# Kernel tuning notes

Measured on AMD Instinct MI355X. Metric: run time of the kernel, lower is better.

## Reference

```python
import jax, jax.numpy as jnp
import numpy as np

NUM_HEADS = 16
NUM_KV_HEADS = 2
HEAD_DIM = 256
HIDDEN = 2048
ROT_DIM = 64          # head_dim * partial_rotary_factor (0.25)
ROPE_THETA = 10000.0
EPS = 1e-6
T = 4096


def setup_inputs() -> dict:
    key = jax.random.key(0)
    k1, k2, k3, k4, k5 = jax.random.split(key, 5)
    qkv_out = HEAD_DIM * (NUM_HEADS * 2 + 2 * NUM_KV_HEADS)  # 9216 (q+gate, k, v)
    return {
        "hidden_states": jax.random.normal(k1, (T, HIDDEN), dtype=jnp.float32),
        "positions": jnp.arange(T, dtype=jnp.int32),
        "w_qkv": jax.random.normal(k2, (HIDDEN, qkv_out), dtype=jnp.float32) * 0.02,
        "w_o": jax.random.normal(k3, (NUM_HEADS * HEAD_DIM, HIDDEN), dtype=jnp.float32) * 0.02,
        "q_norm_w": jax.random.normal(k4, (HEAD_DIM,), dtype=jnp.float32) * 0.1,
        "k_norm_w": jax.random.normal(k5, (HEAD_DIM,), dtype=jnp.float32) * 0.1,
    }


def _gemma_rmsnorm(x, w):
    # GemmaRMSNorm: fp32 compute, scale by (1 + weight)
    xf = x.astype(jnp.float32)
    xf = xf * jax.lax.rsqrt(jnp.mean(xf * xf, axis=-1, keepdims=True) + EPS)
    return (xf * (1.0 + w.astype(jnp.float32))).astype(x.dtype)


def _apply_rope(x, positions):
    # neox-style partial RoPE on first ROT_DIM dims; x: [T, H, D]
    half = ROT_DIM // 2
    inv_freq = 1.0 / (ROPE_THETA ** (jnp.arange(0, ROT_DIM, 2, dtype=jnp.float32) / ROT_DIM))
    freqs = positions.astype(jnp.float32)[:, None] * inv_freq  # [T, half]
    cos = jnp.cos(freqs)[:, None, :]  # [T, 1, half]
    sin = jnp.sin(freqs)[:, None, :]
    x1 = x[..., :half]
    x2 = x[..., half:ROT_DIM]
    rot = jnp.concatenate([x1 * cos - x2 * sin, x2 * cos + x1 * sin], axis=-1)
    return jnp.concatenate([rot, x[..., ROT_DIM:]], axis=-1)


def reference(hidden_states, positions, w_qkv, w_o, q_norm_w, k_norm_w):
    q_size = NUM_HEADS * HEAD_DIM
    kv_size = NUM_KV_HEADS * HEAD_DIM
    qkv = hidden_states @ w_qkv  # [T, 2*q_size + 2*kv_size]

    # split q+gate (interleaved per head), k, v
    q_gate = qkv[:, : 2 * q_size].reshape(-1, NUM_HEADS, 2 * HEAD_DIM)
    q = q_gate[..., :HEAD_DIM]          # [T, H, D]
    gate = q_gate[..., HEAD_DIM:]       # [T, H, D]
    k = qkv[:, 2 * q_size : 2 * q_size + kv_size].reshape(-1, NUM_KV_HEADS, HEAD_DIM)
    v = qkv[:, 2 * q_size + kv_size :].reshape(-1, NUM_KV_HEADS, HEAD_DIM)

    # per-head QK RMSNorm then partial RoPE
    q = _apply_rope(_gemma_rmsnorm(q, q_norm_w), positions)
    k = _apply_rope(_gemma_rmsnorm(k, k_norm_w), positions)

    # GQA causal attention
    rep = NUM_HEADS // NUM_KV_HEADS
    k_rep = jnp.repeat(k, rep, axis=1)  # [T, H, D]
    v_rep = jnp.repeat(v, rep, axis=1)
    scaling = HEAD_DIM ** -0.5
    scores = jnp.einsum("qhd,khd->hqk", q, k_rep) * scaling  # [H, T, T]
    causal = positions[:, None] >= positions[None, :]
    scores = jnp.where(causal[None, :, :], scores, jnp.finfo(scores.dtype).min)
    probs = jax.nn.softmax(scores, axis=-1)
    attn = jnp.einsum("hqk,khd->qhd", probs, v_rep)  # [T, H, D]

    # sigmoid-gated output, then O projection
    attn = attn * jax.nn.sigmoid(gate)
    return attn.reshape(-1, NUM_HEADS * HEAD_DIM) @ w_o
```

## Files before the change

kernel.cpp:

```cpp
#include <hip/hip_runtime.h>

typedef __attribute__((ext_vector_type(4))) float f32x4;
typedef __attribute__((ext_vector_type(8))) __bf16 bf16x8;
typedef unsigned short ushort_t;
typedef unsigned int uint_t;
typedef __attribute__((ext_vector_type(4))) uint_t u32x4;

__device__ __forceinline__ float bf2f(ushort_t u) {
  union { uint_t i; float f; } v; v.i = ((uint_t)u) << 16; return v.f;
}
__device__ __forceinline__ ushort_t f2bf(float f) {
  union { float f; uint_t i; } v; v.f = f;
  uint_t x = v.i;
  return (ushort_t)((x + 0x7fffu + ((x >> 16) & 1u)) >> 16);
}

__device__ __forceinline__ void gload_lds16(const void* g, void* l) {
  __builtin_amdgcn_global_load_lds(
      (const __attribute__((address_space(1))) void*)g,
      (__attribute__((address_space(3))) void*)l, 16, 0, 0);
}

__global__ __launch_bounds__(256) void cast_bf16_kernel(
    const float* __restrict__ in, ushort_t* __restrict__ out, int n8) {
  int i = blockIdx.x * 256 + threadIdx.x;
  if (i >= n8) return;
  float4 a = ((const float4*)in)[i * 2];
  float4 b = ((const float4*)in)[i * 2 + 1];
  ushort4 o0 = make_ushort4(f2bf(a.x), f2bf(a.y), f2bf(a.z), f2bf(a.w));
  ushort4 o1 = make_ushort4(f2bf(b.x), f2bf(b.y), f2bf(b.z), f2bf(b.w));
  ((ushort4*)out)[i * 2] = o0;
  ((ushort4*)out)[i * 2 + 1] = o1;
}

__global__ __launch_bounds__(256) void transpose_cast_kernel(
    const float* __restrict__ in, ushort_t* __restrict__ out, int R, int C) {
  __shared__ float tile[32][33];
  int tx = threadIdx.x, ty = threadIdx.y;
  int c0 = blockIdx.x * 32, r0 = blockIdx.y * 32;
#pragma unroll
  for (int i = 0; i < 4; ++i)
    tile[ty + i * 8][tx] = in[(size_t)(r0 + ty + i * 8) * C + c0 + tx];
  __syncthreads();
#pragma unroll
  for (int i = 0; i < 4; ++i)
    out[(size_t)(c0 + ty + i * 8) * R + r0 + tx] = f2bf(tile[tx][ty + i * 8]);
}

template <int OUT_BF16>
__global__ __launch_bounds__(256, 2) void gemm_bt_kernel(
    const ushort_t* __restrict__ A, const ushort_t* __restrict__ BT,
    void* __restrict__ Cout, int M, int N, int K, int nx, int cpx) {
  const int lin = blockIdx.x;
  const int swz = (lin & 7) * cpx + (lin >> 3);
  const int bx = swz % nx, by = swz / nx;

  __shared__ ushort_t As[128 * 32];
  __shared__ ushort_t Bs[128 * 32];
  const int tid = threadIdx.x;
  const int lane = tid & 63;
  const int wid = tid >> 6;
  const int wr = wid >> 1, wc = wid & 1;
  const int qr = lane & 15, kg = lane >> 4;
  const size_t arow = (size_t)by * 128;
  const size_t brow = (size_t)bx * 128;

  f32x4 acc[4][4] = {};

  for (int k0 = 0; k0 < K; k0 += 32) {
    __syncthreads();
#pragma unroll
    for (int t = 0; t < 2; ++t) {
      int c = (t * 4 + wid) * 64 + lane;
      int r = c >> 2, kc = (c & 3) * 8;
      gload_lds16(A + (arow + r) * K + k0 + kc, &As[(t * 4 + wid) * 512]);
      gload_lds16(BT + (brow + r) * K + k0 + kc, &Bs[(t * 4 + wid) * 512]);
    }
    __syncthreads();
    bf16x8 af[4], bfr[4];
#pragma unroll
    for (int m = 0; m < 4; ++m)
      af[m] = *(const bf16x8*)&As[(wr * 64 + m * 16 + qr) * 32 + kg * 8];
#pragma unroll
    for (int n = 0; n < 4; ++n)
      bfr[n] = *(const bf16x8*)&Bs[(wc * 64 + n * 16 + qr) * 32 + kg * 8];
#pragma unroll
    for (int m = 0; m < 4; ++m)
#pragma unroll
      for (int n = 0; n < 4; ++n)
        acc[m][n] = __builtin_amdgcn_mfma_f32_16x16x32_bf16(af[m], bfr[n], acc[m][n], 0, 0, 0);
  }

#pragma unroll
  for (int m = 0; m < 4; ++m)
#pragma unroll
    for (int n = 0; n < 4; ++n)
#pragma unroll
      for (int j = 0; j < 4; ++j) {
        size_t row = arow + wr * 64 + m * 16 + kg * 4 + j;
        size_t col = brow + wc * 64 + n * 16 + qr;
        float v = acc[m][n][j];
        if (OUT_BF16) ((ushort_t*)Cout)[row * N + col] = f2bf(v);
        else ((float*)Cout)[row * N + col] = v;
      }
}

__global__ __launch_bounds__(256) void normrope_kernel(
    ushort_t* __restrict__ qkv, const int* __restrict__ positions,
    const float* __restrict__ qw, const float* __restrict__ kw) {
  const int wv = blockIdx.x * 4 + (threadIdx.x >> 6);
  const int lane = threadIdx.x & 63;
  const int t = wv / 18;
  const int idx = wv % 18;
  size_t base;
  const float* w;
  float sc;
  if (idx < 16) { base = (size_t)t * 9216 + idx * 512; w = qw; sc = 0.0625f; }
  else { base = (size_t)t * 9216 + 8192 + (size_t)(idx - 16) * 256; w = kw; sc = 1.0f; }

  ushort4 raw = *(const ushort4*)(qkv + base + lane * 4);
  float x0 = bf2f(raw.x), x1 = bf2f(raw.y), x2 = bf2f(raw.z), x3 = bf2f(raw.w);
  float ss = x0 * x0 + x1 * x1 + x2 * x2 + x3 * x3;
#pragma unroll
  for (int off = 1; off < 64; off <<= 1) ss += __shfl_xor(ss, off);
  float inv = rsqrtf(ss * (1.0f / 256.0f) + 1e-6f);
  const int d0 = lane * 4;
  float xn[4] = { x0 * inv * (1.f + w[d0]), x1 * inv * (1.f + w[d0 + 1]),
                  x2 * inv * (1.f + w[d0 + 2]), x3 * inv * (1.f + w[d0 + 3]) };
  float pn[4];
#pragma unroll
  for (int j = 0; j < 4; ++j) pn[j] = __shfl_xor(xn[j], 8);
  if (lane < 16) {
    const float pos = (float)positions[t];
#pragma unroll
    for (int j = 0; j < 4; ++j) {
      int d = d0 + j;
      int i = d & 31;
      float invf = __expf(-(float)i * 0.28782313662425574f);
      float fr = pos * invf;
      float s, c;
      sincosf(fr, &s, &c);
      xn[j] = (d < 32) ? (xn[j] * c - pn[j] * s) : (xn[j] * c + pn[j] * s);
    }
  }
  ushort4 o = make_ushort4(f2bf(xn[0] * sc), f2bf(xn[1] * sc),
                           f2bf(xn[2] * sc), f2bf(xn[3] * sc));
  *(ushort4*)(qkv + base + lane * 4) = o;
}

__device__ __forceinline__ bf16x8 softmax_group(
    f32x4 sA, f32x4 sB, int kv0, int qg, bool full,
    float& mr, float& lr, f32x4* o, int kg) {
  float v[8];
#pragma unroll
  for (int j = 0; j < 4; ++j) v[j] = sA[j];
#pragma unroll
  for (int j = 0; j < 4; ++j) v[4 + j] = sB[j];
  if (!full) {
#pragma unroll
    for (int j = 0; j < 4; ++j) {
      if (kv0 + kg * 4 + j > qg) v[j] = -1e30f;
      if (kv0 + 16 + kg * 4 + j > qg) v[4 + j] = -1e30f;
    }
  }
  float tm = v[0];
#pragma unroll
  for (int j = 1; j < 8; ++j) tm = fmaxf(tm, v[j]);
  tm = fmaxf(tm, __shfl_xor(tm, 16));
  tm = fmaxf(tm, __shfl_xor(tm, 32));
  float mref;
  if (__all(tm - mr <= 8.0f)) {
    mref = mr;
  } else {
    float mnew = fmaxf(mr, tm);
    float corr = __expf(mr - mnew);
    lr *= corr;
    float c0 = __shfl(corr, kg * 4 + 0);
    float c1 = __shfl(corr, kg * 4 + 1);
    float c2 = __shfl(corr, kg * 4 + 2);
    float c3 = __shfl(corr, kg * 4 + 3);
#pragma unroll
    for (int n = 0; n < 16; ++n) {
      o[n][0] *= c0; o[n][1] *= c1; o[n][2] *= c2; o[n][3] *= c3;
    }
    mr = mnew; mref = mnew;
  }
  float p[8];
#pragma unroll
  for (int j = 0; j < 8; ++j) p[j] = __expf(v[j] - mref);
  float ps = 0.f;
#pragma unroll
  for (int j = 0; j < 8; ++j) ps += p[j];
  ps += __shfl_xor(ps, 16);
  ps += __shfl_xor(ps, 32);
  lr += ps;
  union { u32x4 u; bf16x8 b; } pk;
#pragma unroll
  for (int u2 = 0; u2 < 4; ++u2)
    pk.u[u2] = (uint_t)f2bf(p[u2]) | ((uint_t)f2bf(p[4 + u2]) << 16);
  return pk.b;
}

__global__ __launch_bounds__(256, 1) void attn_kernel(
    const ushort_t* __restrict__ qkv, ushort_t* __restrict__ A2) {
  const int id = blockIdx.x;
  const int g8 = id & 255, k8 = id >> 8;
  const int t8 = g8 >> 4;
  const int h = ((g8 & 1) << 3) | ((g8 >> 1) & 7);
  const int qt = k8 ? (15 - t8) : (16 + t8);
  const int kvh = g8 & 1;
  const int tid = threadIdx.x;
  const int lane = tid & 63;
  const int wid = tid >> 6;
  const int qr = lane & 15, kg = lane >> 4;

  __shared__ __align__(16) ushort_t Ks[2][32 * 256];
  __shared__ __align__(16) ushort_t Vt[2][256 * 32];

  const int q0 = qt * 128;
  const int myq0 = q0 + wid * 32;

  bf16x8 qf[2][8];
#pragma unroll
  for (int g = 0; g < 2; ++g)
#pragma unroll
    for (int kd = 0; kd < 8; ++kd)
      qf[g][kd] = *(const bf16x8*)(qkv + (size_t)(myq0 + g * 16 + qr) * 9216 +
                                   h * 512 + kd * 32 + kg * 8);

  f32x4 o0[16] = {}, o1[16] = {};
  float mr0 = -1e30f, mr1 = -1e30f, lr0 = 0.f, lr1 = 0.f;

  const int nt = qt * 4 + 4;

  u32x4 vlo0, vhi0, vlo1, vhi1;
  const int vr = tid & 15;
  const int vd0 = (tid >> 4) * 8;
  const int vd1 = vd0 + 128;

#pragma unroll
  for (int t = 0; t < 4; ++t) {
    int c = (t * 4 + wid) * 64 + lane;
    int r = c >> 5, dc = c & 31;
    int dcs = dc ^ (r & 7);
    gload_lds16(qkv + (size_t)r * 9216 + 8192 + kvh * 256 + dcs * 8,
                &Ks[0][(t * 4 + wid) * 512]);
  }
  {
    const ushort_t* g0 = qkv + (size_t)vr * 9216 + 8704 + kvh * 256;
    vlo0 = *(const u32x4*)(g0 + vd0);
    vhi0 = *(const u32x4*)(g0 + 16 * 9216 + vd0);
    vlo1 = *(const u32x4*)(g0 + vd1);
    vhi1 = *(const u32x4*)(g0 + 16 * 9216 + vd1);
  }

  int buf = 0;
  for (int kt = 0; kt < nt; ++kt) {
    const int kv0 = kt * 32;

    {
      char* vbase = (char*)&Vt[buf][0];
#pragma unroll
      for (int half = 0; half < 2; ++half) {
        u32x4 lo = half ? vlo1 : vlo0;
        u32x4 hi = half ? vhi1 : vhi0;
        int dbase = half ? vd1 : vd0;
#pragma unroll
        for (int w = 0; w < 4; ++w) {
          uint_t v0 = (lo[w] & 0xffffu) | (hi[w] << 16);
          uint_t v1 = (lo[w] >> 16) | (hi[w] & 0xffff0000u);
          int d0v = dbase + 2 * w, d1v = d0v + 1;
          int rsw = ((vr >> 2) * 16) + (vr & 3) * 4;
          *(uint_t*)(vbase + (d0v ^ ((d0v >> 3) & 1)) * 64 +
                     (rsw ^ ((d0v & 3) * 16))) = v0;
          *(uint_t*)(vbase + (d1v ^ ((d1v >> 3) & 1)) * 64 +
                     (rsw ^ ((d1v & 3) * 16))) = v1;
        }
      }
    }
    __syncthreads();

    if (kt + 1 < nt) {
      const int kv0n = kv0 + 32;
#pragma unroll
      for (int t = 0; t < 4; ++t) {
        int c = (t * 4 + wid) * 64 + lane;
        int r = c >> 5, dc = c & 31;
        int dcs = dc ^ (r & 7);
        gload_lds16(qkv + (size_t)(kv0n + r) * 9216 + 8192 + kvh * 256 + dcs * 8,
                    &Ks[buf ^ 1][(t * 4 + wid) * 512]);
      }
      const ushort_t* g0 = qkv + (size_t)(kv0n + vr) * 9216 + 8704 + kvh * 256;
      vlo0 = *(const u32x4*)(g0 + vd0);
      vhi0 = *(const u32x4*)(g0 + 16 * 9216 + vd0);
      vlo1 = *(const u32x4*)(g0 + vd1);
      vhi1 = *(const u32x4*)(g0 + 16 * 9216 + vd1);
    }
    __builtin_amdgcn_sched_barrier(0);

    const bool active = (kv0 <= myq0 + 31);
    if (active) {
      const char* ksb = (const char*)&Ks[buf][0];
      const int kxor = (qr & 7) << 4;
      const int kbase = qr * 512;
      f32x4 s00 = {0.f, 0.f, 0.f, 0.f}, s01 = {0.f, 0.f, 0.f, 0.f};
      f32x4 s10 = {0.f, 0.f, 0.f, 0.f}, s11 = {0.f, 0.f, 0.f, 0.f};
      __builtin_amdgcn_s_setprio(1);
#pragma unroll
      for (int kd = 0; kd < 8; ++kd) {
        int off = kbase + ((kd * 64 + kg * 16) ^ kxor);
        bf16x8 kf0 = *(const bf16x8*)(ksb + off);
        bf16x8 kf1 = *(const bf16x8*)(ksb + off + 8192);
        s00 = __builtin_amdgcn_mfma_f32_16x16x32_bf16(kf0, qf[0][kd], s00, 0, 0, 0);
        s01 = __builtin_amdgcn_mfma_f32_16x16x32_bf16(kf0, qf[1][kd], s01, 0, 0, 0);
        s10 = __builtin_amdgcn_mfma_f32_16x16x32_bf16(kf1, qf[0][kd], s10, 0, 0, 0);
        s11 = __builtin_amdgcn_mfma_f32_16x16x32_bf16(kf1, qf[1][kd], s11, 0, 0, 0);
      }
      __builtin_amdgcn_s_setprio(0);

      const bool full = (kv0 + 31 <= myq0);
      bf16x8 pf0 = softmax_group(s00, s10, kv0, myq0 + qr, full, mr0, lr0, o0, kg);
      bf16x8 pf1 = softmax_group(s01, s11, kv0, myq0 + 16 + qr, full, mr1, lr1, o1, kg);

      const char* vtb = (const char*)&Vt[buf][0];
      __builtin_amdgcn_s_setprio(1);
#pragma unroll
      for (int n = 0; n < 16; ++n) {
        int dcol = n * 16 + qr;
        int dsw = dcol ^ ((dcol >> 3) & 1);
        bf16x8 vf = *(const bf16x8*)(vtb + dsw * 64 + ((kg ^ (dcol & 3)) * 16));
        o0[n] = __builtin_amdgcn_mfma_f32_16x16x32_bf16(pf0, vf, o0[n], 0, 0, 0);
        o1[n] = __builtin_amdgcn_mfma_f32_16x16x32_bf16(pf1, vf, o1[n], 0, 0, 0);
      }
      __builtin_amdgcn_s_setprio(0);
    }
    buf ^= 1;
  }

  float rl0[4], rl1[4];
#pragma unroll
  for (int j = 0; j < 4; ++j) {
    rl0[j] = 1.0f / __shfl(lr0, kg * 4 + j);
    rl1[j] = 1.0f / __shfl(lr1, kg * 4 + j);
  }
#pragma unroll
  for (int n = 0; n < 16; ++n) {
    int d = n * 16 + qr;
#pragma unroll
    for (int j = 0; j < 4; ++j) {
      {
        int t = myq0 + kg * 4 + j;
        float val = o0[n][j] * rl0[j];
        float g2 = bf2f(qkv[(size_t)t * 9216 + h * 512 + 256 + d]);
        val *= 1.0f / (1.0f + __expf(-g2));
        A2[(size_t)t * 4096 + h * 256 + d] = f2bf(val);
      }
      {
        int t = myq0 + 16 + kg * 4 + j;
        float val = o1[n][j] * rl1[j];
        float g2 = bf2f(qkv[(size_t)t * 9216 + h * 512 + 256 + d]);
        val *= 1.0f / (1.0f + __expf(-g2));
        A2[(size_t)t * 4096 + h * 256 + d] = f2bf(val);
      }
    }
  }
}

extern "C" void kernel_launch(void* const* d_in, const int* in_sizes, int n_in,
                              void* d_out, int out_size, void* d_ws, size_t ws_size,
                              hipStream_t stream) {
  const float* hidden = (const float*)d_in[0];
  const int* positions = (const int*)d_in[1];
  const float* w_qkv = (const float*)d_in[2];
  const float* w_o = (const float*)d_in[3];
  const float* q_norm_w = (const float*)d_in[4];
  const float* k_norm_w = (const float*)d_in[5];

  char* ws = (char*)d_ws;
  ushort_t* hb    = (ushort_t*)ws;
  ushort_t* wqkvT = (ushort_t*)(ws + 16777216);
  ushort_t* woT   = (ushort_t*)(ws + 54525952);
  ushort_t* qkvb  = (ushort_t*)(ws + 71303168);
  ushort_t* A2    = (ushort_t*)(ws + 146800640);

  hipLaunchKernelGGL(cast_bf16_kernel, dim3(4096), dim3(256), 0, stream,
                     hidden, hb, 1048576);
  hipLaunchKernelGGL(transpose_cast_kernel, dim3(288, 64), dim3(32, 8), 0, stream,
                     w_qkv, wqkvT, 2048, 9216);
  hipLaunchKernelGGL(transpose_cast_kernel, dim3(64, 128), dim3(32, 8), 0, stream,
                     w_o, woT, 4096, 2048);
  hipLaunchKernelGGL((gemm_bt_kernel<1>), dim3(2304), dim3(256), 0, stream,
                     hb, wqkvT, (void*)qkvb, 4096, 9216, 2048, 72, 288);
  hipLaunchKernelGGL(normrope_kernel, dim3(18432), dim3(256), 0, stream,
                     qkvb, positions, q_norm_w, k_norm_w);
  hipLaunchKernelGGL(attn_kernel, dim3(512), dim3(256), 0, stream,
                     qkvb, A2);
  hipLaunchKernelGGL((gemm_bt_kernel<0>), dim3(512), dim3(256), 0, stream,
                     A2, woT, d_out, 4096, 2048, 4096, 16, 64);
}
```

Before: 738.0 us.

## Halve attention query tile to raise occupancy and single-buffer V in LDS

Measured after the change: 913.9 us. 1.24x slower.

```diff
diff --git a/kernel.cpp b/kernel.cpp
--- a/kernel.cpp
+++ b/kernel.cpp
@@ -201,13 +201,13 @@
   return pk.b;
 }
 
-__global__ __launch_bounds__(256, 1) void attn_kernel(
+__global__ __launch_bounds__(256, 3) void attn_kernel(
     const ushort_t* __restrict__ qkv, ushort_t* __restrict__ A2) {
   const int id = blockIdx.x;
-  const int g8 = id & 255, k8 = id >> 8;
-  const int t8 = g8 >> 4;
+  const int g8 = id & 255, kk = id >> 8;
+  const int x = g8 >> 4;
   const int h = ((g8 & 1) << 3) | ((g8 >> 1) & 7);
-  const int qt = k8 ? (15 - t8) : (16 + t8);
+  const int qt = (3 - kk) * 16 + ((kk & 1) ? (15 - x) : x);
   const int kvh = g8 & 1;
   const int tid = threadIdx.x;
   const int lane = tid & 63;
@@ -215,23 +215,21 @@
   const int qr = lane & 15, kg = lane >> 4;
 
   __shared__ __align__(16) ushort_t Ks[2][32 * 256];
-  __shared__ __align__(16) ushort_t Vt[2][256 * 32];
-
-  const int q0 = qt * 128;
-  const int myq0 = q0 + wid * 32;
-
-  bf16x8 qf[2][8];
-#pragma unroll
-  for (int g = 0; g < 2; ++g)
-#pragma unroll
-    for (int kd = 0; kd < 8; ++kd)
-      qf[g][kd] = *(const bf16x8*)(qkv + (size_t)(myq0 + g * 16 + qr) * 9216 +
-                                   h * 512 + kd * 32 + kg * 8);
-
-  f32x4 o0[16] = {}, o1[16] = {};
-  float mr0 = -1e30f, mr1 = -1e30f, lr0 = 0.f, lr1 = 0.f;
-
-  const int nt = qt * 4 + 4;
+  __shared__ __align__(16) ushort_t Vt[256 * 32];
+
+  const int q0 = qt * 64;
+  const int myq0 = q0 + wid * 16;
+
+  bf16x8 qf[8];
+#pragma unroll
+  for (int kd = 0; kd < 8; ++kd)
+    qf[kd] = *(const bf16x8*)(qkv + (size_t)(myq0 + qr) * 9216 + h * 512 +
+                              kd * 32 + kg * 8);
+
+  f32x4 o[16] = {};
+  float mr = -1e30f, lr = 0.f;
+
+  const int nt = qt * 2 + 2;
 
   u32x4 vlo0, vhi0, vlo1, vhi1;
   const int vr = tid & 15;
@@ -259,7 +257,7 @@
     const int kv0 = kt * 32;
 
     {
-      char* vbase = (char*)&Vt[buf][0];
+      char* vbase = (char*)&Vt[0];
 #pragma unroll
       for (int half = 0; half < 2; ++half) {
         u32x4 lo = half ? vlo1 : vlo0;
@@ -298,70 +296,54 @@
     }
     __builtin_amdgcn_sched_barrier(0);
 
-    const bool active = (kv0 <= myq0 + 31);
+    const bool active = (kv0 <= myq0 + 15);
     if (active) {
       const char* ksb = (const char*)&Ks[buf][0];
       const int kxor = (qr & 7) << 4;
       const int kbase = qr * 512;
-      f32x4 s00 = {0.f, 0.f, 0.f, 0.f}, s01 = {0.f, 0.f, 0.f, 0.f};
-      f32x4 s10 = {0.f, 0.f, 0.f, 0.f}, s11 = {0.f, 0.f, 0.f, 0.f};
+      f32x4 s0 = {0.f, 0.f, 0.f, 0.f}, s1 = {0.f, 0.f, 0.f, 0.f};
       __builtin_amdgcn_s_setprio(1);
 #pragma unroll
       for (int kd = 0; kd < 8; ++kd) {
         int off = kbase + ((kd * 64 + kg * 16) ^ kxor);
         bf16x8 kf0 = *(const bf16x8*)(ksb + off);
         bf16x8 kf1 = *(const bf16x8*)(ksb + off + 8192);
-        s00 = __builtin_amdgcn_mfma_f32_16x16x32_bf16(kf0, qf[0][kd], s00, 0, 0, 0);
-        s01 = __builtin_amdgcn_mfma_f32_16x16x32_bf16(kf0, qf[1][kd], s01, 0, 0, 0);
-        s10 = __builtin_amdgcn_mfma_f32_16x16x32_bf16(kf1, qf[0][kd], s10, 0, 0, 0);
-        s11 = __builtin_amdgcn_mfma_f32_16x16x32_bf16(kf1, qf[1][kd], s11, 0, 0, 0);
+        s0 = __builtin_amdgcn_mfma_f32_16x16x32_bf16(kf0, qf[kd], s0, 0, 0, 0);
+        s1 = __builtin_amdgcn_mfma_f32_16x16x32_bf16(kf1, qf[kd], s1, 0, 0, 0);
       }
       __builtin_amdgcn_s_setprio(0);
 
       const bool full = (kv0 + 31 <= myq0);
-      bf16x8 pf0 = softmax_group(s00, s10, kv0, myq0 + qr, full, mr0, lr0, o0, kg);
-      bf16x8 pf1 = softmax_group(s01, s11, kv0, myq0 + 16 + qr, full, mr1, lr1, o1, kg);
-
-      const char* vtb = (const char*)&Vt[buf][0];
+      bf16x8 pf = softmax_group(s0, s1, kv0, myq0 + qr, full, mr, lr, o, kg);
+
+      const char* vtb = (const char*)&Vt[0];
       __builtin_amdgcn_s_setprio(1);
 #pragma unroll
       for (int n = 0; n < 16; ++n) {
         int dcol = n * 16 + qr;
         int dsw = dcol ^ ((dcol >> 3) & 1);
         bf16x8 vf = *(const bf16x8*)(vtb + dsw * 64 + ((kg ^ (dcol & 3)) * 16));
-        o0[n] = __builtin_amdgcn_mfma_f32_16x16x32_bf16(pf0, vf, o0[n], 0, 0, 0);
-        o1[n] = __builtin_amdgcn_mfma_f32_16x16x32_bf16(pf1, vf, o1[n], 0, 0, 0);
+        o[n] = __builtin_amdgcn_mfma_f32_16x16x32_bf16(pf, vf, o[n], 0, 0, 0);
       }
       __builtin_amdgcn_s_setprio(0);
     }
+    __syncthreads();
     buf ^= 1;
   }
 
-  float rl0[4], rl1[4];
-#pragma unroll
-  for (int j = 0; j < 4; ++j) {
-    rl0[j] = 1.0f / __shfl(lr0, kg * 4 + j);
-    rl1[j] = 1.0f / __shfl(lr1, kg * 4 + j);
-  }
+  float rl[4];
+#pragma unroll
+  for (int j = 0; j < 4; ++j) rl[j] = 1.0f / __shfl(lr, kg * 4 + j);
 #pragma unroll
   for (int n = 0; n < 16; ++n) {
     int d = n * 16 + qr;
 #pragma unroll
     for (int j = 0; j < 4; ++j) {
-      {
-        int t = myq0 + kg * 4 + j;
-        float val = o0[n][j] * rl0[j];
-        float g2 = bf2f(qkv[(size_t)t * 9216 + h * 512 + 256 + d]);
-        val *= 1.0f / (1.0f + __expf(-g2));
-        A2[(size_t)t * 4096 + h * 256 + d] = f2bf(val);
-      }
-      {
-        int t = myq0 + 16 + kg * 4 + j;
-        float val = o1[n][j] * rl1[j];
-        float g2 = bf2f(qkv[(size_t)t * 9216 + h * 512 + 256 + d]);
-        val *= 1.0f / (1.0f + __expf(-g2));
-        A2[(size_t)t * 4096 + h * 256 + d] = f2bf(val);
-      }
+      int t = myq0 + kg * 4 + j;
+      float val = o[n][j] * rl[j];
+      float g2 = bf2f(qkv[(size_t)t * 9216 + h * 512 + 256 + d]);
+      val *= 1.0f / (1.0f + __expf(-g2));
+      A2[(size_t)t * 4096 + h * 256 + d] = f2bf(val);
     }
   }
 }
@@ -393,7 +375,7 @@
                      hb, wqkvT, (void*)qkvb, 4096, 9216, 2048, 72, 288);
   hipLaunchKernelGGL(normrope_kernel, dim3(18432), dim3(256), 0, stream,
                      qkvb, positions, q_norm_w, k_norm_w);
-  hipLaunchKernelGGL(attn_kernel, dim3(512), dim3(256), 0, stream,
+  hipLaunchKernelGGL(attn_kernel, dim3(1024), dim3(256), 0, stream,
                      qkvb, A2);
   hipLaunchKernelGGL((gemm_bt_kernel<0>), dim3(512), dim3(256), 0, stream,
                      A2, woT, d_out, 4096, 2048, 4096, 16, 64);
```
